# Kernel tuning notes

Hardware: AMD Instinct MI355X
Metric: run time of the kernel (lower is better)

## Reference

```python
import jax, jax.numpy as jnp
import numpy as np

N_SAMPLES = 4000
K = 20            # n_neighbors
E = 172           # node feature dim = embed_dim
DE = 172          # edge feature dim (kdim = vdim = E + DE)
H = 2             # n_heads
N_NODES = 100000
N_EDGES = 500000
N_LAYERS = 2


def setup_inputs() -> dict:
    key = jax.random.key(0)
    ks = jax.random.split(key, 16)
    s = 0.05
    return {
        'nodes': jax.random.randint(ks[0], (3 * N_SAMPLES,), 0, N_NODES),
        'timestamps': jax.random.uniform(ks[1], (3 * N_SAMPLES,), jnp.float32) * 1000.0,
        'neighbors': jax.random.randint(ks[2], (3 * N_SAMPLES, K), 0, N_NODES),
        'edge_idxs_nb': jax.random.randint(ks[3], (3 * N_SAMPLES, K), 0, N_EDGES),
        'node_features': jax.random.normal(ks[4], (N_NODES, E), jnp.float32) * s,
        'edge_features': jax.random.normal(ks[5], (N_EDGES, DE), jnp.float32) * s,
        'time_w': jax.random.normal(ks[6], (E,), jnp.float32),
        'time_b': jax.random.normal(ks[7], (E,), jnp.float32),
        'q_w': jax.random.normal(ks[8], (E, E), jnp.float32) * s,
        'k_w': jax.random.normal(ks[9], (E, E + DE), jnp.float32) * s,
        'v_w': jax.random.normal(ks[10], (E, E + DE), jnp.float32) * s,
        'bq': jnp.zeros((E,), jnp.float32),
        'bk': jnp.zeros((E,), jnp.float32),
        'bv': jnp.zeros((E,), jnp.float32),
        'out_w': jax.random.normal(ks[11], (E, E), jnp.float32) * s,
        'out_b': jnp.zeros((E,), jnp.float32),
    }


def _time_encode(t, w, b):
    # TGAT-style time encoder: cos(t * w + b), t: [...], out: [..., E]
    return jnp.cos(t[..., None] * w + b)


def _mha(q_in, kv, pad_mask, q_w, k_w, v_w, bq, bk, bv, out_w, out_b):
    # q_in: [B, E], kv: [B, K, E+DE], pad_mask: [B, K] bool (True = masked)
    B = q_in.shape[0]
    hd = E // H
    q = (q_in @ q_w.T + bq).reshape(B, H, hd)            # [B,H,hd]
    k = (kv @ k_w.T + bk).reshape(B, K, H, hd)            # [B,K,H,hd]
    v = (kv @ v_w.T + bv).reshape(B, K, H, hd)
    scores = jnp.einsum('bhd,bkhd->bhk', q, k) / np.sqrt(hd)
    scores = jnp.where(pad_mask[:, None, :], -1e9, scores)
    attn = jax.nn.softmax(scores, axis=-1)                # dropout inactive (eval)
    out = jnp.einsum('bhk,bkhd->bhd', attn, v).reshape(B, E)
    return out @ out_w.T + out_b


def reference(nodes, timestamps, neighbors, edge_idxs_nb, node_features,
              edge_features, time_w, time_b, q_w, k_w, v_w, bq, bk, bv,
              out_w, out_b):
    # key padding mask from raw neighbor ids (0 = padding); fix all-masked rows
    pad = neighbors == 0                                  # [3N, K]
    invalid = jnp.all(pad, axis=1, keepdims=True)
    pad = pad & ~(invalid & (jnp.arange(K) == 0))

    t = _time_encode(timestamps, time_w, time_b)          # [3N, E]
    t_nb = t[:, None, :]                                  # repeated per neighbor

    nf = node_features
    h = nf[nodes]                                         # [3N, E]
    for i in range(N_LAYERS):
        if i != 0:
            nf = nf.at[nodes].set(h)                      # scatter update
            h = nf[nodes]
        q_in = h + t                                      # Fuse
        hn = nf[neighbors]                                # [3N, K, E] gather
        ef = edge_features[edge_idxs_nb]                  # [3N, K, DE]
        kv = jnp.concatenate([hn + t_nb, ef], axis=-1)    # [3N, K, E+DE]
        h = _mha(q_in, kv, pad, q_w, k_w, v_w, bq, bk, bv, out_w, out_b)

    n = N_SAMPLES
    return (h[:n], h[n:2 * n], h[2 * n:])
```

## Files before the change

### kernel.cpp

```cpp
#include <hip/hip_runtime.h>
#include <hip/hip_bf16.h>


#define NSMP   12000
#define KNB    20
#define EDIM   172
#define HDIM   86
#define NNODES 100000
#define NT_N   11
#define KS_N   6
#define TBL_SZ (NT_N * KS_N * 64 * 8)

typedef unsigned int uint;
typedef unsigned short ushort;
typedef __attribute__((ext_vector_type(8))) short  bf16x8;
typedef __attribute__((ext_vector_type(4))) float  f32x4;

static __device__ __forceinline__ ushort f2bf(float f) {
    uint u = __float_as_uint(f);
    uint r = (u + 0x7fffu + ((u >> 16) & 1u)) >> 16;
    return (ushort)r;
}
static __device__ __forceinline__ float bf2f(ushort b) {
    return __uint_as_float(((uint)b) << 16);
}

__global__ __launch_bounds__(256) void time_enc_kernel(
    const float* __restrict__ ts, const float* __restrict__ tw,
    const float* __restrict__ tb, float* __restrict__ t)
{
    int i = blockIdx.x * 256 + threadIdx.x;
    if (i < NSMP * EDIM) {
        int b = i / EDIM, e = i - b * EDIM;
        t[i] = cosf(ts[b] * tw[e] + tb[e]);
    }
}

__global__ __launch_bounds__(256) void winner_init_kernel(int* __restrict__ w)
{
    int i = blockIdx.x * 256 + threadIdx.x;
    if (i < NNODES) w[i] = -1;
}
__global__ __launch_bounds__(256) void winner_scatter_kernel(
    const int* __restrict__ nodes, int* __restrict__ w)
{
    int i = blockIdx.x * 256 + threadIdx.x;
    if (i < NSMP) atomicMax(&w[nodes[i]], i);
}

__global__ __launch_bounds__(256) void preswizzle_kernel(
    const float* __restrict__ q_w, const float* __restrict__ out_w,
    const float* __restrict__ k_w, const float* __restrict__ v_w,
    ushort* __restrict__ BF)
{
    int gid = blockIdx.x * 256 + threadIdx.x;
    int total = 6 * NT_N * KS_N * 64;
    if (gid >= total) return;
    int tbl  = gid / (NT_N * KS_N * 64);
    int rem  = gid - tbl * (NT_N * KS_N * 64);
    int lane = rem & 63;
    int fs   = rem >> 6;
    int s    = fs % KS_N;
    int nt   = fs / KS_N;

    const float* src; int ldb, koff;
    switch (tbl) {
        case 0: src = q_w;   ldb = EDIM;     koff = 0;    break;
        case 1: src = out_w; ldb = EDIM;     koff = 0;    break;
        case 2: src = k_w;   ldb = 2 * EDIM; koff = 0;    break;
        case 3: src = k_w;   ldb = 2 * EDIM; koff = EDIM; break;
        case 4: src = v_w;   ldb = 2 * EDIM; koff = 0;    break;
        default: src = v_w;  ldb = 2 * EDIM; koff = EDIM; break;
    }
    int n  = nt * 16 + (lane & 15);
    int k0 = s * 32 + (lane >> 4) * 8;
    ushort* dst = BF + (size_t)tbl * TBL_SZ + (size_t)(fs * 64 + lane) * 8;
    #pragma unroll
    for (int j = 0; j < 8; j++) {
        int k = k0 + j;
        dst[j] = (n < EDIM && k < EDIM) ? f2bf(src[(long)n * ldb + koff + k]) : (ushort)0;
    }
}

__global__ __launch_bounds__(256) void gemm_rf_kernel(
    const float* __restrict__ A, const int* __restrict__ Aidx, int M,
    const ushort* __restrict__ BF1, const ushort* __restrict__ BF2,
    const float* __restrict__ bias1, const float* __restrict__ bias2,
    float* __restrict__ C1f, ushort* __restrict__ C1h,
    float* __restrict__ C2f, ushort* __restrict__ C2h)
{
    const int lane = threadIdx.x & 63;
    const int wave = threadIdx.x >> 6;
    const int col  = lane & 15;
    const int quad = lane >> 4;
    const int m0   = blockIdx.x * 64 + wave * 16;
    if (m0 >= M) return;
    const bool dual = (BF2 != nullptr);

    long arow = m0 + col;
    if (Aidx) arow = (long)Aidx[arow];
    const float* ap = A + arow * EDIM + quad * 8;

    bf16x8 af[KS_N];
    #pragma unroll
    for (int s = 0; s < KS_N - 1; s++) {
        float4 f0 = *(const float4*)(ap + s * 32);
        float4 f1 = *(const float4*)(ap + s * 32 + 4);
        af[s][0] = f2bf(f0.x); af[s][1] = f2bf(f0.y);
        af[s][2] = f2bf(f0.z); af[s][3] = f2bf(f0.w);
        af[s][4] = f2bf(f1.x); af[s][5] = f2bf(f1.y);
        af[s][6] = f2bf(f1.z); af[s][7] = f2bf(f1.w);
    }
    {
        const int kb = 160 + quad * 8;
        #pragma unroll
        for (int j = 0; j < 8; j++)
            af[KS_N - 1][j] = (kb + j < EDIM) ? f2bf(ap[160 + j]) : (short)0;
    }

    #pragma unroll
    for (int nt = 0; nt < NT_N; nt++) {
        const ushort* bp1 = BF1 + (size_t)(nt * KS_N * 64 + lane) * 8;
        bf16x8 bf1[KS_N];
        #pragma unroll
        for (int s = 0; s < KS_N; s++)
            bf1[s] = *(const bf16x8*)(bp1 + (size_t)s * 64 * 8);
        f32x4 acc1 = {0.f, 0.f, 0.f, 0.f};
        f32x4 acc2 = {0.f, 0.f, 0.f, 0.f};
        if (dual) {
            const ushort* bp2 = BF2 + (size_t)(nt * KS_N * 64 + lane) * 8;
            bf16x8 bf2[KS_N];
            #pragma unroll
            for (int s = 0; s < KS_N; s++)
                bf2[s] = *(const bf16x8*)(bp2 + (size_t)s * 64 * 8);
            #pragma unroll
            for (int s = 0; s < KS_N; s++) {
                acc1 = __builtin_amdgcn_mfma_f32_16x16x32_bf16(af[s], bf1[s], acc1, 0, 0, 0);
                acc2 = __builtin_amdgcn_mfma_f32_16x16x32_bf16(af[s], bf2[s], acc2, 0, 0, 0);
            }
        } else {
            #pragma unroll
            for (int s = 0; s < KS_N; s++)
                acc1 = __builtin_amdgcn_mfma_f32_16x16x32_bf16(af[s], bf1[s], acc1, 0, 0, 0);
        }

        const int n = nt * 16 + col;
        if (n < EDIM) {
            const float bb1 = bias1 ? bias1[n] : 0.f;
            #pragma unroll
            for (int r = 0; r < 4; r++) {
                long ci = (long)(m0 + quad * 4 + r) * EDIM + n;
                float v1 = acc1[r] + bb1;
                if (C1f) C1f[ci] = v1; else C1h[ci] = f2bf(v1);
            }
            if (dual) {
                const float bb2 = bias2 ? bias2[n] : 0.f;
                #pragma unroll
                for (int r = 0; r < 4; r++) {
                    long ci = (long)(m0 + quad * 4 + r) * EDIM + n;
                    float v2 = acc2[r] + bb2;
                    if (C2f) C2f[ci] = v2; else C2h[ci] = f2bf(v2);
                }
            }
        }
    }
}

#define SKP 176

__global__ __launch_bounds__(256) void attn_kernel(
    const int* __restrict__ neighbors,
    const float* __restrict__ TQ, const float* __restrict__ TV,
    const float* __restrict__ HQ,
    const int* __restrict__ nodes, const int* __restrict__ winner,
    const ushort* __restrict__ NodeK, const ushort* __restrict__ NodeV,
    const float* __restrict__ H1K, const float* __restrict__ H1V,
    const ushort* __restrict__ EfK, const ushort* __restrict__ EfV,
    float* __restrict__ attn_out)
{
    const int b = blockIdx.x;
    const int t = threadIdx.x;
    __shared__ float sq[SKP];
    __shared__ float sk[KNB * SKP];
    __shared__ float sv[KNB * SKP];
    __shared__ float sw[2][KNB];
    __shared__ int   snb[KNB];
    __shared__ int   spad[KNB];

    if (t < KNB) {
        int nb = neighbors[b * KNB + t];
        snb[t]  = nb;
        spad[t] = (nb == 0) ? 1 : 0;
    }
    if (t < EDIM) {
        float q;
        if (winner) {
            int j = winner[nodes[b]];
            q = HQ[(long)j * EDIM + t] + TQ[(long)b * EDIM + t];
        } else {
            q = HQ[(long)b * EDIM + t] + TQ[(long)b * EDIM + t];
        }
        sq[t] = q;
    }
    __syncthreads();
    if (t == 0) {
        int c = 0;
        for (int k = 0; k < KNB; k++) c += spad[k];
        if (c == KNB) spad[0] = 0;
    }

    for (int task = t; task < KNB * 43; task += 256) {
        int kk = task / 43, c = task - kk * 43;
        int e  = c * 4;
        int nb = snb[kk];
        float4 kv, vv;
        bool l2 = false;
        if (winner) {
            int w = winner[nb];
            if (w >= 0) {
                kv = *(const float4*)(H1K + (long)w * EDIM + e);
                vv = *(const float4*)(H1V + (long)w * EDIM + e);
                l2 = true;
            }
        }
        if (!l2) {
            ushort4 kb4 = *(const ushort4*)(NodeK + (long)nb * EDIM + e);
            ushort4 vb4 = *(const ushort4*)(NodeV + (long)nb * EDIM + e);
            kv = make_float4(bf2f(kb4.x), bf2f(kb4.y), bf2f(kb4.z), bf2f(kb4.w));
            vv = make_float4(bf2f(vb4.x), bf2f(vb4.y), bf2f(vb4.z), bf2f(vb4.w));
        }
        long eoff = ((long)b * KNB + kk) * EDIM + e;
        ushort4 ek = *(const ushort4*)(EfK + eoff);
        ushort4 ev = *(const ushort4*)(EfV + eoff);
        float* skp = &sk[kk * SKP + e];
        float* svp = &sv[kk * SKP + e];
        skp[0] = kv.x + bf2f(ek.x); skp[1] = kv.y + bf2f(ek.y);
        skp[2] = kv.z + bf2f(ek.z); skp[3] = kv.w + bf2f(ek.w);
        svp[0] = vv.x + bf2f(ev.x); svp[1] = vv.y + bf2f(ev.y);
        svp[2] = vv.z + bf2f(ev.z); svp[3] = vv.w + bf2f(ev.w);
    }
    __syncthreads();

    if (t < 2 * KNB * 4) {
        int kk = t >> 3, h = (t >> 2) & 1, part = t & 3;
        int d0 = part * 22, d1 = d0 + 22; if (d1 > HDIM) d1 = HDIM;
        const float* qp = &sq[h * HDIM];
        const float* kp = &sk[kk * SKP + h * HDIM];
        float s = 0.f;
        for (int d = d0; d < d1; d++) s += qp[d] * kp[d];
        s += __shfl_xor(s, 1, 64);
        s += __shfl_xor(s, 2, 64);
        if (part == 0)
            sw[h][kk] = spad[kk] ? -1e9f : (s * 0.10783277320343841f);
    }
    __syncthreads();
    if (t < 2) {
        float mx = -1e30f;
        for (int kk = 0; kk < KNB; kk++) mx = fmaxf(mx, sw[t][kk]);
        float sum = 0.f, ex[KNB];
        for (int kk = 0; kk < KNB; kk++) { ex[kk] = expf(sw[t][kk] - mx); sum += ex[kk]; }
        float inv = 1.f / sum;
        for (int kk = 0; kk < KNB; kk++) sw[t][kk] = ex[kk] * inv;
    }
    __syncthreads();
    if (t < EDIM) {
        int h = t / HDIM;
        float acc = 0.f;
        for (int kk = 0; kk < KNB; kk++) acc += sw[h][kk] * sv[kk * SKP + t];
        attn_out[(long)b * EDIM + t] = acc + TV[(long)b * EDIM + t];
    }
}

extern "C" void kernel_launch(void* const* d_in, const int* in_sizes, int n_in,
                              void* d_out, int out_size, void* d_ws, size_t ws_size,
                              hipStream_t stream)
{
    const int*   nodes   = (const int*)d_in[0];
    const float* ts      = (const float*)d_in[1];
    const int*   neigh   = (const int*)d_in[2];
    const int*   edgeidx = (const int*)d_in[3];
    const float* nodef   = (const float*)d_in[4];
    const float* edgef   = (const float*)d_in[5];
    const float* time_w  = (const float*)d_in[6];
    const float* time_b  = (const float*)d_in[7];
    const float* q_w     = (const float*)d_in[8];
    const float* k_w     = (const float*)d_in[9];
    const float* v_w     = (const float*)d_in[10];
    const float* bq      = (const float*)d_in[11];
    const float* bv      = (const float*)d_in[13];
    const float* out_w   = (const float*)d_in[14];
    const float* out_b   = (const float*)d_in[15];
    float* out = (float*)d_out;

    char* wsp = (char*)d_ws;
    size_t off = 0;
    auto alloc = [&](size_t bytes) -> void* {
        void* p = wsp + off;
        off += (bytes + 255) & ~(size_t)255;
        return p;
    };
    const size_t SE = (size_t)NSMP * EDIM;
    float* t_enc = (float*)alloc(SE * 4);
    float* TQ    = (float*)alloc(SE * 4);
    float* TV    = (float*)alloc(SE * 4);
    float* HQ    = (float*)alloc(SE * 4);
    float* AO    = (float*)alloc(SE * 4);
    float* H1    = (float*)alloc(SE * 4);
    float* H1Q   = (float*)alloc(SE * 4);
    float* H1K   = (float*)alloc(SE * 4);
    float* H1V   = (float*)alloc(SE * 4);
    int*   winner = (int*)alloc((size_t)NNODES * 4);
    ushort* NodeK = (ushort*)alloc((size_t)NNODES * EDIM * 2);
    ushort* NodeV = (ushort*)alloc((size_t)NNODES * EDIM * 2);
    ushort* EfK   = (ushort*)alloc((size_t)NSMP * KNB * EDIM * 2);
    ushort* EfV   = (ushort*)alloc((size_t)NSMP * KNB * EDIM * 2);
    ushort* BF    = (ushort*)alloc((size_t)6 * TBL_SZ * 2);
    if (off > ws_size) return;

    const ushort* BFq   = BF + 0 * TBL_SZ;
    const ushort* BFout = BF + 1 * TBL_SZ;
    const ushort* BFkE  = BF + 2 * TBL_SZ;
    const ushort* BFkDE = BF + 3 * TBL_SZ;
    const ushort* BFvE  = BF + 4 * TBL_SZ;
    const ushort* BFvDE = BF + 5 * TBL_SZ;

    dim3 blk(256);
    const int gS = (NSMP + 63) / 64;

    preswizzle_kernel<<<(6 * NT_N * KS_N * 64 + 255) / 256, blk, 0, stream>>>(
        q_w, out_w, k_w, v_w, BF);
    time_enc_kernel<<<(NSMP * EDIM + 255) / 256, blk, 0, stream>>>(ts, time_w, time_b, t_enc);

    gemm_rf_kernel<<<gS, blk, 0, stream>>>(t_enc, nullptr, NSMP,
        BFq, BFvE, bq, bv, TQ, nullptr, TV, nullptr);
    gemm_rf_kernel<<<(NNODES + 63) / 64, blk, 0, stream>>>(nodef, nullptr, NNODES,
        BFkE, BFvE, nullptr, nullptr, nullptr, NodeK, nullptr, NodeV);
    gemm_rf_kernel<<<(NSMP * KNB + 63) / 64, blk, 0, stream>>>(edgef, edgeidx, NSMP * KNB,
        BFkDE, BFvDE, nullptr, nullptr, nullptr, EfK, nullptr, EfV);
    gemm_rf_kernel<<<gS, blk, 0, stream>>>(nodef, nodes, NSMP,
        BFq, nullptr, nullptr, nullptr, HQ, nullptr, nullptr, nullptr);

    attn_kernel<<<NSMP, blk, 0, stream>>>(neigh, TQ, TV, HQ,
        nullptr, nullptr, NodeK, NodeV, nullptr, nullptr, EfK, EfV, AO);
    gemm_rf_kernel<<<gS, blk, 0, stream>>>(AO, nullptr, NSMP,
        BFout, nullptr, out_b, nullptr, H1, nullptr, nullptr, nullptr);

    winner_init_kernel<<<(NNODES + 255) / 256, blk, 0, stream>>>(winner);
    winner_scatter_kernel<<<(NSMP + 255) / 256, blk, 0, stream>>>(nodes, winner);

    gemm_rf_kernel<<<gS, blk, 0, stream>>>(H1, nullptr, NSMP,
        BFq, nullptr, nullptr, nullptr, H1Q, nullptr, nullptr, nullptr);
    gemm_rf_kernel<<<gS, blk, 0, stream>>>(H1, nullptr, NSMP,
        BFkE, BFvE, nullptr, nullptr, H1K, nullptr, H1V, nullptr);

    attn_kernel<<<NSMP, blk, 0, stream>>>(neigh, TQ, TV, H1Q,
        nodes, winner, NodeK, NodeV, H1K, H1V, EfK, EfV, AO);
    gemm_rf_kernel<<<gS, blk, 0, stream>>>(AO, nullptr, NSMP,
        BFout, nullptr, out_b, nullptr, out, nullptr, nullptr, nullptr);
}
```

Before: 956.9 us.

## Fold edge-feature projections into query-side and output-side weights to skip per-edge GEMMs

Stops projecting the 240k gathered edge-feature rows through the K and V DE-blocks. The query is instead premultiplied by the transposed K edge weights per head (QT0/QT1), and attention-weighted raw edge features are aggregated and pushed through precomputed out_w·V_DE matrices in a fused three-way output GEMM. The node GEMM now processes four row blocks per wave so B fragments are reused. The attention kernel reads K/V directly from global memory instead of staging them in shared memory, and it adds extra dot products and larger per-sample outputs.

```diff
diff --git a/kernel.cpp b/kernel.cpp
--- a/kernel.cpp
+++ b/kernel.cpp
@@ -1,5 +1,4 @@
 #include <hip/hip_runtime.h>
-#include <hip/hip_bf16.h>
 
 
 #define NSMP   12000
@@ -9,7 +8,9 @@
 #define NNODES 100000
 #define NT_N   11
 #define KS_N   6
+#define NTBL   8
 #define TBL_SZ (NT_N * KS_N * 64 * 8)
+#define SKP    176
 
 typedef unsigned int uint;
 typedef unsigned short ushort;
@@ -25,6 +26,25 @@
     return __uint_as_float(((uint)b) << 16);
 }
 
+static __device__ __forceinline__ void load_afrag(
+    const float* __restrict__ rowp, int quad, bf16x8* af)
+{
+    const float* ap = rowp + quad * 8;
+    #pragma unroll
+    for (int s = 0; s < KS_N - 1; s++) {
+        float4 f0 = *(const float4*)(ap + s * 32);
+        float4 f1 = *(const float4*)(ap + s * 32 + 4);
+        af[s][0] = f2bf(f0.x); af[s][1] = f2bf(f0.y);
+        af[s][2] = f2bf(f0.z); af[s][3] = f2bf(f0.w);
+        af[s][4] = f2bf(f1.x); af[s][5] = f2bf(f1.y);
+        af[s][6] = f2bf(f1.z); af[s][7] = f2bf(f1.w);
+    }
+    const int kt = EDIM - 160 - quad * 8;
+    #pragma unroll
+    for (int j = 0; j < 8; j++)
+        af[KS_N - 1][j] = (j < kt) ? (short)f2bf(ap[160 + j]) : (short)0;
+}
+
 __global__ __launch_bounds__(256) void time_enc_kernel(
     const float* __restrict__ ts, const float* __restrict__ tw,
     const float* __restrict__ tb, float* __restrict__ t)
@@ -47,14 +67,37 @@
     int i = blockIdx.x * 256 + threadIdx.x;
     if (i < NSMP) atomicMax(&w[nodes[i]], i);
 }
+__global__ __launch_bounds__(256) void jmap_kernel(
+    const int* __restrict__ nodes, const int* __restrict__ w,
+    int* __restrict__ jmap)
+{
+    int i = blockIdx.x * 256 + threadIdx.x;
+    if (i < NSMP) jmap[i] = w[nodes[i]];
+}
+
+__global__ __launch_bounds__(256) void mcompute_kernel(
+    const float* __restrict__ out_w, const float* __restrict__ v_w,
+    float* __restrict__ Mbuf)
+{
+    int idx = blockIdx.x * 256 + threadIdx.x;
+    if (idx >= 2 * EDIM * EDIM) return;
+    int h = idx / (EDIM * EDIM);
+    int r = idx - h * (EDIM * EDIM);
+    int i = r / EDIM, j = r - i * EDIM;
+    float s = 0.f;
+    for (int d = 0; d < HDIM; d++)
+        s += out_w[i * EDIM + h * HDIM + d] *
+             v_w[(long)(h * HDIM + d) * (2 * EDIM) + EDIM + j];
+    Mbuf[idx] = s;
+}
 
 __global__ __launch_bounds__(256) void preswizzle_kernel(
     const float* __restrict__ q_w, const float* __restrict__ out_w,
     const float* __restrict__ k_w, const float* __restrict__ v_w,
-    ushort* __restrict__ BF)
+    const float* __restrict__ Mbuf, ushort* __restrict__ BF)
 {
     int gid = blockIdx.x * 256 + threadIdx.x;
-    int total = 6 * NT_N * KS_N * 64;
+    int total = NTBL * NT_N * KS_N * 64;
     if (gid >= total) return;
     int tbl  = gid / (NT_N * KS_N * 64);
     int rem  = gid - tbl * (NT_N * KS_N * 64);
@@ -62,30 +105,35 @@
     int fs   = rem >> 6;
     int s    = fs % KS_N;
     int nt   = fs / KS_N;
-
-    const float* src; int ldb, koff;
-    switch (tbl) {
-        case 0: src = q_w;   ldb = EDIM;     koff = 0;    break;
-        case 1: src = out_w; ldb = EDIM;     koff = 0;    break;
-        case 2: src = k_w;   ldb = 2 * EDIM; koff = 0;    break;
-        case 3: src = k_w;   ldb = 2 * EDIM; koff = EDIM; break;
-        case 4: src = v_w;   ldb = 2 * EDIM; koff = 0;    break;
-        default: src = v_w;  ldb = 2 * EDIM; koff = EDIM; break;
-    }
-    int n  = nt * 16 + (lane & 15);
-    int k0 = s * 32 + (lane >> 4) * 8;
+    int n    = nt * 16 + (lane & 15);
+    int k0   = s * 32 + (lane >> 4) * 8;
     ushort* dst = BF + (size_t)tbl * TBL_SZ + (size_t)(fs * 64 + lane) * 8;
     #pragma unroll
     for (int j = 0; j < 8; j++) {
         int k = k0 + j;
-        dst[j] = (n < EDIM && k < EDIM) ? f2bf(src[(long)n * ldb + koff + k]) : (ushort)0;
-    }
-}
-
+        float val = 0.f;
+        if (n < EDIM && k < EDIM) {
+            switch (tbl) {
+                case 0: val = q_w[(long)n * EDIM + k]; break;
+                case 1: val = out_w[(long)n * EDIM + k]; break;
+                case 2: val = k_w[(long)n * 2 * EDIM + k]; break;
+                case 3: val = v_w[(long)n * 2 * EDIM + k]; break;
+                case 4: val = (k <  HDIM) ? k_w[(long)k * 2 * EDIM + EDIM + n] : 0.f; break;
+                case 5: val = (k >= HDIM) ? k_w[(long)k * 2 * EDIM + EDIM + n] : 0.f; break;
+                case 6: val = Mbuf[(long)n * EDIM + k]; break;
+                default: val = Mbuf[(long)EDIM * EDIM + (long)n * EDIM + k]; break;
+            }
+        }
+        dst[j] = f2bf(val);
+    }
+}
+
+template<int RB>
 __global__ __launch_bounds__(256) void gemm_rf_kernel(
     const float* __restrict__ A, const int* __restrict__ Aidx, int M,
     const ushort* __restrict__ BF1, const ushort* __restrict__ BF2,
     const float* __restrict__ bias1, const float* __restrict__ bias2,
+    const float* __restrict__ add1,
     float* __restrict__ C1f, ushort* __restrict__ C1h,
     float* __restrict__ C2f, ushort* __restrict__ C2h)
 {
@@ -93,151 +141,156 @@
     const int wave = threadIdx.x >> 6;
     const int col  = lane & 15;
     const int quad = lane >> 4;
-    const int m0   = blockIdx.x * 64 + wave * 16;
+    const int m0   = (blockIdx.x * 4 + wave) * (16 * RB);
     if (m0 >= M) return;
     const bool dual = (BF2 != nullptr);
 
-    long arow = m0 + col;
-    if (Aidx) arow = (long)Aidx[arow];
-    const float* ap = A + arow * EDIM + quad * 8;
-
-    bf16x8 af[KS_N];
-    #pragma unroll
-    for (int s = 0; s < KS_N - 1; s++) {
-        float4 f0 = *(const float4*)(ap + s * 32);
-        float4 f1 = *(const float4*)(ap + s * 32 + 4);
-        af[s][0] = f2bf(f0.x); af[s][1] = f2bf(f0.y);
-        af[s][2] = f2bf(f0.z); af[s][3] = f2bf(f0.w);
-        af[s][4] = f2bf(f1.x); af[s][5] = f2bf(f1.y);
-        af[s][6] = f2bf(f1.z); af[s][7] = f2bf(f1.w);
-    }
-    {
-        const int kb = 160 + quad * 8;
-        #pragma unroll
-        for (int j = 0; j < 8; j++)
-            af[KS_N - 1][j] = (kb + j < EDIM) ? f2bf(ap[160 + j]) : (short)0;
+    bf16x8 af[RB][KS_N];
+    bool rv[RB];
+    #pragma unroll
+    for (int rb = 0; rb < RB; rb++) {
+        int mr = m0 + rb * 16;
+        rv[rb] = (mr < M);
+        long arow = rv[rb] ? (long)(mr + col) : 0;
+        if (Aidx) arow = (long)Aidx[arow];
+        load_afrag(A + arow * EDIM, quad, af[rb]);
     }
 
     #pragma unroll
     for (int nt = 0; nt < NT_N; nt++) {
         const ushort* bp1 = BF1 + (size_t)(nt * KS_N * 64 + lane) * 8;
-        bf16x8 bf1[KS_N];
+        const ushort* bp2 = dual ? BF2 + (size_t)(nt * KS_N * 64 + lane) * 8 : bp1;
+        f32x4 acc1[RB], acc2[RB];
         #pragma unroll
-        for (int s = 0; s < KS_N; s++)
-            bf1[s] = *(const bf16x8*)(bp1 + (size_t)s * 64 * 8);
-        f32x4 acc1 = {0.f, 0.f, 0.f, 0.f};
-        f32x4 acc2 = {0.f, 0.f, 0.f, 0.f};
-        if (dual) {
-            const ushort* bp2 = BF2 + (size_t)(nt * KS_N * 64 + lane) * 8;
-            bf16x8 bf2[KS_N];
+        for (int rb = 0; rb < RB; rb++) {
+            acc1[rb] = {0.f, 0.f, 0.f, 0.f};
+            acc2[rb] = {0.f, 0.f, 0.f, 0.f};
+        }
+        #pragma unroll
+        for (int s = 0; s < KS_N; s++) {
+            bf16x8 b1 = *(const bf16x8*)(bp1 + (size_t)s * 64 * 8);
             #pragma unroll
-            for (int s = 0; s < KS_N; s++)
-                bf2[s] = *(const bf16x8*)(bp2 + (size_t)s * 64 * 8);
-            #pragma unroll
-            for (int s = 0; s < KS_N; s++) {
-                acc1 = __builtin_amdgcn_mfma_f32_16x16x32_bf16(af[s], bf1[s], acc1, 0, 0, 0);
-                acc2 = __builtin_amdgcn_mfma_f32_16x16x32_bf16(af[s], bf2[s], acc2, 0, 0, 0);
+            for (int rb = 0; rb < RB; rb++)
+                acc1[rb] = __builtin_amdgcn_mfma_f32_16x16x32_bf16(af[rb][s], b1, acc1[rb], 0, 0, 0);
+            if (dual) {
+                bf16x8 b2 = *(const bf16x8*)(bp2 + (size_t)s * 64 * 8);
+                #pragma unroll
+                for (int rb = 0; rb < RB; rb++)
+                    acc2[rb] = __builtin_amdgcn_mfma_f32_16x16x32_bf16(af[rb][s], b2, acc2[rb], 0, 0, 0);
             }
-        } else {
-            #pragma unroll
-            for (int s = 0; s < KS_N; s++)
-                acc1 = __builtin_amdgcn_mfma_f32_16x16x32_bf16(af[s], bf1[s], acc1, 0, 0, 0);
-        }
-
+        }
         const int n = nt * 16 + col;
         if (n < EDIM) {
             const float bb1 = bias1 ? bias1[n] : 0.f;
+            const float bb2 = bias2 ? bias2[n] : 0.f;
+            #pragma unroll
+            for (int rb = 0; rb < RB; rb++) {
+                if (!rv[rb]) continue;
+                #pragma unroll
+                for (int r = 0; r < 4; r++) {
+                    long ci = (long)(m0 + rb * 16 + quad * 4 + r) * EDIM + n;
+                    float v1 = acc1[rb][r] + bb1;
+                    if (add1) v1 += add1[ci];
+                    if (C1f) C1f[ci] = v1; else C1h[ci] = f2bf(v1);
+                    if (dual) {
+                        float v2 = acc2[rb][r] + bb2;
+                        if (C2f) C2f[ci] = v2; else C2h[ci] = f2bf(v2);
+                    }
+                }
+            }
+        }
+    }
+}
+
+__global__ __launch_bounds__(256) void gemm_out3_kernel(
+    const float* __restrict__ A1,
+    const float* __restrict__ A2,
+    int M,
+    const ushort* __restrict__ BFo, const ushort* __restrict__ BFm0,
+    const ushort* __restrict__ BFm1,
+    const float* __restrict__ bias, float* __restrict__ C)
+{
+    const int lane = threadIdx.x & 63;
+    const int wave = threadIdx.x >> 6;
+    const int col  = lane & 15;
+    const int quad = lane >> 4;
+    const int m0   = (blockIdx.x * 4 + wave) * 16;
+    if (m0 >= M) return;
+    const long arow = m0 + col;
+
+    bf16x8 afo[KS_N], afa[KS_N], afb[KS_N];
+    load_afrag(A1 + arow * EDIM, quad, afo);
+    load_afrag(A2 + arow * 2 * EDIM, quad, afa);
+    load_afrag(A2 + arow * 2 * EDIM + EDIM, quad, afb);
+
+    #pragma unroll
+    for (int nt = 0; nt < NT_N; nt++) {
+        const ushort* bpo = BFo  + (size_t)(nt * KS_N * 64 + lane) * 8;
+        const ushort* bp0 = BFm0 + (size_t)(nt * KS_N * 64 + lane) * 8;
+        const ushort* bp1 = BFm1 + (size_t)(nt * KS_N * 64 + lane) * 8;
+        f32x4 acc = {0.f, 0.f, 0.f, 0.f};
+        #pragma unroll
+        for (int s = 0; s < KS_N; s++) {
+            bf16x8 bo = *(const bf16x8*)(bpo + (size_t)s * 64 * 8);
+            acc = __builtin_amdgcn_mfma_f32_16x16x32_bf16(afo[s], bo, acc, 0, 0, 0);
+            bf16x8 b0 = *(const bf16x8*)(bp0 + (size_t)s * 64 * 8);
+            acc = __builtin_amdgcn_mfma_f32_16x16x32_bf16(afa[s], b0, acc, 0, 0, 0);
+            bf16x8 b1 = *(const bf16x8*)(bp1 + (size_t)s * 64 * 8);
+            acc = __builtin_amdgcn_mfma_f32_16x16x32_bf16(afb[s], b1, acc, 0, 0, 0);
+        }
+        const int n = nt * 16 + col;
+        if (n < EDIM) {
+            const float bb = bias ? bias[n] : 0.f;
             #pragma unroll
             for (int r = 0; r < 4; r++) {
                 long ci = (long)(m0 + quad * 4 + r) * EDIM + n;
-                float v1 = acc1[r] + bb1;
-                if (C1f) C1f[ci] = v1; else C1h[ci] = f2bf(v1);
+                C[ci] = acc[r] + bb;
             }
-            if (dual) {
-                const float bb2 = bias2 ? bias2[n] : 0.f;
-                #pragma unroll
-                for (int r = 0; r < 4; r++) {
-                    long ci = (long)(m0 + quad * 4 + r) * EDIM + n;
-                    float v2 = acc2[r] + bb2;
-                    if (C2f) C2f[ci] = v2; else C2h[ci] = f2bf(v2);
-                }
-            }
-        }
-    }
-}
-
-#define SKP 176
+        }
+    }
+}
 
 __global__ __launch_bounds__(256) void attn_kernel(
-    const int* __restrict__ neighbors,
-    const float* __restrict__ TQ, const float* __restrict__ TV,
-    const float* __restrict__ HQ,
-    const int* __restrict__ nodes, const int* __restrict__ winner,
+    const int* __restrict__ neighbors, const int* __restrict__ eidx,
+    const float* __restrict__ Q, const float* __restrict__ QT0,
+    const float* __restrict__ QT1, const float* __restrict__ TV,
+    const float* __restrict__ edgef,
+    const int* __restrict__ winner,
     const ushort* __restrict__ NodeK, const ushort* __restrict__ NodeV,
     const float* __restrict__ H1K, const float* __restrict__ H1V,
-    const ushort* __restrict__ EfK, const ushort* __restrict__ EfV,
-    float* __restrict__ attn_out)
+    float* __restrict__ AO, float* __restrict__ AGG)
 {
     const int b = blockIdx.x;
     const int t = threadIdx.x;
-    __shared__ float sq[SKP];
-    __shared__ float sk[KNB * SKP];
-    __shared__ float sv[KNB * SKP];
+    __shared__ float sq[SKP], sq0[SKP], sq1[SKP];
+    __shared__ float sef[KNB * SKP];
     __shared__ float sw[2][KNB];
-    __shared__ int   snb[KNB];
-    __shared__ int   spad[KNB];
+    __shared__ int   snb[KNB], sei[KNB], swin[KNB], spad[KNB];
 
     if (t < KNB) {
         int nb = neighbors[b * KNB + t];
         snb[t]  = nb;
         spad[t] = (nb == 0) ? 1 : 0;
+        sei[t]  = eidx[b * KNB + t];
     }
     if (t < EDIM) {
-        float q;
-        if (winner) {
-            int j = winner[nodes[b]];
-            q = HQ[(long)j * EDIM + t] + TQ[(long)b * EDIM + t];
-        } else {
-            q = HQ[(long)b * EDIM + t] + TQ[(long)b * EDIM + t];
-        }
-        sq[t] = q;
+        sq[t]  = Q[(long)b * EDIM + t];
+        sq0[t] = QT0[(long)b * EDIM + t];
+        sq1[t] = QT1[(long)b * EDIM + t];
     }
     __syncthreads();
+
+    if (t < KNB) swin[t] = winner ? winner[snb[t]] : -1;
     if (t == 0) {
         int c = 0;
         for (int k = 0; k < KNB; k++) c += spad[k];
         if (c == KNB) spad[0] = 0;
     }
-
     for (int task = t; task < KNB * 43; task += 256) {
-        int kk = task / 43, c = task - kk * 43;
-        int e  = c * 4;
-        int nb = snb[kk];
-        float4 kv, vv;
-        bool l2 = false;
-        if (winner) {
-            int w = winner[nb];
-            if (w >= 0) {
-                kv = *(const float4*)(H1K + (long)w * EDIM + e);
-                vv = *(const float4*)(H1V + (long)w * EDIM + e);
-                l2 = true;
-            }
-        }
-        if (!l2) {
-            ushort4 kb4 = *(const ushort4*)(NodeK + (long)nb * EDIM + e);
-            ushort4 vb4 = *(const ushort4*)(NodeV + (long)nb * EDIM + e);
-            kv = make_float4(bf2f(kb4.x), bf2f(kb4.y), bf2f(kb4.z), bf2f(kb4.w));
-            vv = make_float4(bf2f(vb4.x), bf2f(vb4.y), bf2f(vb4.z), bf2f(vb4.w));
-        }
-        long eoff = ((long)b * KNB + kk) * EDIM + e;
-        ushort4 ek = *(const ushort4*)(EfK + eoff);
-        ushort4 ev = *(const ushort4*)(EfV + eoff);
-        float* skp = &sk[kk * SKP + e];
-        float* svp = &sv[kk * SKP + e];
-        skp[0] = kv.x + bf2f(ek.x); skp[1] = kv.y + bf2f(ek.y);
-        skp[2] = kv.z + bf2f(ek.z); skp[3] = kv.w + bf2f(ek.w);
-        svp[0] = vv.x + bf2f(ev.x); svp[1] = vv.y + bf2f(ev.y);
-        svp[2] = vv.z + bf2f(ev.z); svp[3] = vv.w + bf2f(ev.w);
+        int kk = task / 43, c = task - kk * 43, e = c * 4;
+        float4 ef4 = *(const float4*)(edgef + (long)sei[kk] * EDIM + e);
+        float* p = &sef[kk * SKP + e];
+        p[0] = ef4.x; p[1] = ef4.y; p[2] = ef4.z; p[3] = ef4.w;
     }
     __syncthreads();
 
@@ -245,9 +298,19 @@
         int kk = t >> 3, h = (t >> 2) & 1, part = t & 3;
         int d0 = part * 22, d1 = d0 + 22; if (d1 > HDIM) d1 = HDIM;
         const float* qp = &sq[h * HDIM];
-        const float* kp = &sk[kk * SKP + h * HDIM];
         float s = 0.f;
-        for (int d = d0; d < d1; d++) s += qp[d] * kp[d];
+        int w = swin[kk];
+        if (w >= 0) {
+            const float* kp = H1K + (long)w * EDIM + h * HDIM;
+            for (int d = d0; d < d1; d++) s += qp[d] * kp[d];
+        } else {
+            const ushort* kp = NodeK + (long)snb[kk] * EDIM + h * HDIM;
+            for (int d = d0; d < d1; d++) s += qp[d] * bf2f(kp[d]);
+        }
+        const float* qt = h ? sq1 : sq0;
+        const float* ep = &sef[kk * SKP];
+        int i0 = part * 43;
+        for (int i = i0; i < i0 + 43; i++) s += qt[i] * ep[i];
         s += __shfl_xor(s, 1, 64);
         s += __shfl_xor(s, 2, 64);
         if (part == 0)
@@ -265,9 +328,20 @@
     __syncthreads();
     if (t < EDIM) {
         int h = t / HDIM;
-        float acc = 0.f;
-        for (int kk = 0; kk < KNB; kk++) acc += sw[h][kk] * sv[kk * SKP + t];
-        attn_out[(long)b * EDIM + t] = acc + TV[(long)b * EDIM + t];
+        float acc = 0.f, a0 = 0.f, a1 = 0.f;
+        for (int kk = 0; kk < KNB; kk++) {
+            float w0 = sw[0][kk], w1 = sw[1][kk];
+            int w = swin[kk];
+            float vv = (w >= 0) ? H1V[(long)w * EDIM + t]
+                                : bf2f(NodeV[(long)snb[kk] * EDIM + t]);
+            acc += (h ? w1 : w0) * vv;
+            float ev = sef[kk * SKP + t];
+            a0 += w0 * ev;
+            a1 += w1 * ev;
+        }
+        AO[(long)b * EDIM + t] = acc + TV[(long)b * EDIM + t];
+        AGG[(long)b * 2 * EDIM + t] = a0;
+        AGG[(long)b * 2 * EDIM + EDIM + t] = a1;
     }
 }
 
@@ -303,58 +377,65 @@
     float* t_enc = (float*)alloc(SE * 4);
     float* TQ    = (float*)alloc(SE * 4);
     float* TV    = (float*)alloc(SE * 4);
-    float* HQ    = (float*)alloc(SE * 4);
+    float* Qb    = (float*)alloc(SE * 4);
+    float* QT0   = (float*)alloc(SE * 4);
+    float* QT1   = (float*)alloc(SE * 4);
     float* AO    = (float*)alloc(SE * 4);
     float* H1    = (float*)alloc(SE * 4);
-    float* H1Q   = (float*)alloc(SE * 4);
     float* H1K   = (float*)alloc(SE * 4);
     float* H1V   = (float*)alloc(SE * 4);
+    float* AGG   = (float*)alloc((size_t)NSMP * 2 * EDIM * 4);
+    float* Mbuf  = (float*)alloc((size_t)2 * EDIM * EDIM * 4);
     int*   winner = (int*)alloc((size_t)NNODES * 4);
+    int*   jmap   = (int*)alloc((size_t)NSMP * 4);
     ushort* NodeK = (ushort*)alloc((size_t)NNODES * EDIM * 2);
     ushort* NodeV = (ushort*)alloc((size_t)NNODES * EDIM * 2);
-    ushort* EfK   = (ushort*)alloc((size_t)NSMP * KNB * EDIM * 2);
-    ushort* EfV   = (ushort*)alloc((size_t)NSMP * KNB * EDIM * 2);
-    ushort* BF    = (ushort*)alloc((size_t)6 * TBL_SZ * 2);
+    ushort* BF    = (ushort*)alloc((size_t)NTBL * TBL_SZ * 2);
     if (off > ws_size) return;
 
     const ushort* BFq   = BF + 0 * TBL_SZ;
     const ushort* BFout = BF + 1 * TBL_SZ;
     const ushort* BFkE  = BF + 2 * TBL_SZ;
-    const ushort* BFkDE = BF + 3 * TBL_SZ;
-    const ushort* BFvE  = BF + 4 * TBL_SZ;
-    const ushort* BFvDE = BF + 5 * TBL_SZ;
+    const ushort* BFvE  = BF + 3 * TBL_SZ;
+    const ushort* BFW0  = BF + 4 * TBL_SZ;
+    const ushort* BFW1  = BF + 5 * TBL_SZ;
+    const ushort* BFM0  = BF + 6 * TBL_SZ;
+    const ushort* BFM1  = BF + 7 * TBL_SZ;
 
     dim3 blk(256);
     const int gS = (NSMP + 63) / 64;
 
-    preswizzle_kernel<<<(6 * NT_N * KS_N * 64 + 255) / 256, blk, 0, stream>>>(
-        q_w, out_w, k_w, v_w, BF);
-    time_enc_kernel<<<(NSMP * EDIM + 255) / 256, blk, 0, stream>>>(ts, time_w, time_b, t_enc);
-
-    gemm_rf_kernel<<<gS, blk, 0, stream>>>(t_enc, nullptr, NSMP,
-        BFq, BFvE, bq, bv, TQ, nullptr, TV, nullptr);
-    gemm_rf_kernel<<<(NNODES + 63) / 64, blk, 0, stream>>>(nodef, nullptr, NNODES,
-        BFkE, BFvE, nullptr, nullptr, nullptr, NodeK, nullptr, NodeV);
-    gemm_rf_kernel<<<(NSMP * KNB + 63) / 64, blk, 0, stream>>>(edgef, edgeidx, NSMP * KNB,
-        BFkDE, BFvDE, nullptr, nullptr, nullptr, EfK, nullptr, EfV);
-    gemm_rf_kernel<<<gS, blk, 0, stream>>>(nodef, nodes, NSMP,
-        BFq, nullptr, nullptr, nullptr, HQ, nullptr, nullptr, nullptr);
-
-    attn_kernel<<<NSMP, blk, 0, stream>>>(neigh, TQ, TV, HQ,
-        nullptr, nullptr, NodeK, NodeV, nullptr, nullptr, EfK, EfV, AO);
-    gemm_rf_kernel<<<gS, blk, 0, stream>>>(AO, nullptr, NSMP,
-        BFout, nullptr, out_b, nullptr, H1, nullptr, nullptr, nullptr);
-
     winner_init_kernel<<<(NNODES + 255) / 256, blk, 0, stream>>>(winner);
     winner_scatter_kernel<<<(NSMP + 255) / 256, blk, 0, stream>>>(nodes, winner);
-
-    gemm_rf_kernel<<<gS, blk, 0, stream>>>(H1, nullptr, NSMP,
-        BFq, nullptr, nullptr, nullptr, H1Q, nullptr, nullptr, nullptr);
-    gemm_rf_kernel<<<gS, blk, 0, stream>>>(H1, nullptr, NSMP,
-        BFkE, BFvE, nullptr, nullptr, H1K, nullptr, H1V, nullptr);
-
-    attn_kernel<<<NSMP, blk, 0, stream>>>(neigh, TQ, TV, H1Q,
-        nodes, winner, NodeK, NodeV, H1K, H1V, EfK, EfV, AO);
-    gemm_rf_kernel<<<gS, blk, 0, stream>>>(AO, nullptr, NSMP,
-        BFout, nullptr, out_b, nullptr, out, nullptr, nullptr, nullptr);
-}
+    mcompute_kernel<<<(2 * EDIM * EDIM + 255) / 256, blk, 0, stream>>>(out_w, v_w, Mbuf);
+    preswizzle_kernel<<<(NTBL * NT_N * KS_N * 64 + 255) / 256, blk, 0, stream>>>(
+        q_w, out_w, k_w, v_w, Mbuf, BF);
+    time_enc_kernel<<<(NSMP * EDIM + 255) / 256, blk, 0, stream>>>(ts, time_w, time_b, t_enc);
+
+    gemm_rf_kernel<1><<<gS, blk, 0, stream>>>(t_enc, nullptr, NSMP,
+        BFq, BFvE, bq, bv, nullptr, TQ, nullptr, TV, nullptr);
+    gemm_rf_kernel<4><<<(NNODES + 255) / 256, blk, 0, stream>>>(nodef, nullptr, NNODES,
+        BFkE, BFvE, nullptr, nullptr, nullptr, nullptr, NodeK, nullptr, NodeV);
+    gemm_rf_kernel<1><<<gS, blk, 0, stream>>>(nodef, nodes, NSMP,
+        BFq, nullptr, nullptr, nullptr, TQ, Qb, nullptr, nullptr, nullptr);
+    gemm_rf_kernel<1><<<gS, blk, 0, stream>>>(Qb, nullptr, NSMP,
+        BFW0, BFW1, nullptr, nullptr, nullptr, QT0, nullptr, QT1, nullptr);
+
+    attn_kernel<<<NSMP, blk, 0, stream>>>(neigh, edgeidx, Qb, QT0, QT1, TV,
+        edgef, nullptr, NodeK, NodeV, nullptr, nullptr, AO, AGG);
+    gemm_out3_kernel<<<gS, blk, 0, stream>>>(AO, AGG, NSMP,
+        BFout, BFM0, BFM1, out_b, H1);
+
+    jmap_kernel<<<(NSMP + 255) / 256, blk, 0, stream>>>(nodes, winner, jmap);
+    gemm_rf_kernel<1><<<gS, blk, 0, stream>>>(H1, nullptr, NSMP,
+        BFkE, BFvE, nullptr, nullptr, nullptr, H1K, nullptr, H1V, nullptr);
+    gemm_rf_kernel<1><<<gS, blk, 0, stream>>>(H1, jmap, NSMP,
+        BFq, nullptr, nullptr, nullptr, TQ, Qb, nullptr, nullptr, nullptr);
+    gemm_rf_kernel<1><<<gS, blk, 0, stream>>>(Qb, nullptr, NSMP,
+        BFW0, BFW1, nullptr, nullptr, nullptr, QT0, nullptr, QT1, nullptr);
+
+    attn_kernel<<<NSMP, blk, 0, stream>>>(neigh, edgeidx, Qb, QT0, QT1, TV,
+        edgef, winner, NodeK, NodeV, H1K, H1V, AO, AGG);
+    gemm_out3_kernel<<<gS, blk, 0, stream>>>(AO, AGG, NSMP,
+        BFout, BFM0, BFM1, out_b, out);
+}
```

After: 1.345 ms. +40.5%, slower.
